# Kernel optimization log

Measured on AMD Instinct MI355X. Metric: run time of the kernel, lower is better.

Reference implementation:

```python
import jax, jax.numpy as jnp
import numpy as np

BATCH = 4
N_CTX = 1024
D_IN = 512
N_HEADS = 8
D_HEAD = 64
N_VARS = D_IN // D_HEAD  # ConstrainedRead default: n_vars = d_in // d_var = 8
TEMP = 1.0
ATTN_TEMP = float(np.sqrt(D_HEAD))  # attention_temp default = sqrt(d_head)


def setup_inputs() -> dict:
    key = jax.random.key(0)
    k1, k2, k3, k4, k5 = jax.random.split(key, 5)
    x = jax.random.uniform(k1, (BATCH, N_CTX, D_IN), dtype=jnp.float32)
    # causal tril mask, broadcast to batch (matches registered tril buffer usage)
    mask = jnp.broadcast_to(jnp.tril(jnp.ones((N_CTX, N_CTX), dtype=bool)), (BATCH, N_CTX, N_CTX))
    inv_sv = 1.0 / np.sqrt(N_VARS)
    W_K_W = jax.random.normal(k2, (N_HEADS, N_VARS), dtype=jnp.float32) * inv_sv
    W_Q_W = jax.random.normal(k3, (N_HEADS, N_VARS), dtype=jnp.float32) * inv_sv
    W_V_W = jax.random.normal(k4, (N_HEADS, N_VARS), dtype=jnp.float32) * inv_sv
    W_pred_W = jax.random.normal(k5, (N_HEADS, D_HEAD, D_HEAD), dtype=jnp.float32) / np.sqrt(D_HEAD)
    return {"x": x, "mask": mask, "W_K_W": W_K_W, "W_Q_W": W_Q_W, "W_V_W": W_V_W, "W_pred_W": W_pred_W}


def _constrained_read(W):
    # softmax over variables, then block-diagonal-style selector: (h, d_head, d_in)
    probs = jax.nn.softmax(W / TEMP, axis=-1)                 # (h, n_vars)
    eye = jnp.eye(D_HEAD, dtype=probs.dtype)                  # (c, c)
    rm = probs[:, :, None, None] * eye                        # (h, v, c, c)
    # einops 'a b c d -> a d (b c)'
    return jnp.transpose(rm, (0, 3, 1, 2)).reshape(N_HEADS, D_HEAD, D_IN)


def _fixed_bias_table():
    M = N_CTX  # table layout: [-2, linspace(0,-M,M-1)/M, linspace(-M,0,M)/M], shared over heads
    return jnp.concatenate([
        jnp.array([-2.0], dtype=jnp.float32),
        (jnp.linspace(0.0, -float(M), M - 1) / M).astype(jnp.float32),
        (jnp.linspace(-float(M), 0.0, M) / M).astype(jnp.float32),
    ])  # (2M,)


def reference(x, mask, W_K_W, W_Q_W, W_V_W, W_pred_W):
    WK = _constrained_read(W_K_W)
    WQm = _constrained_read(W_Q_W)
    WV = _constrained_read(W_V_W)
    # WPred: out[h,f,d] = sum_e W_Q[h,e,d] * softmax(W)[h,e,f]
    Wp = jax.nn.softmax(W_pred_W / TEMP, axis=-1)
    WQ = jnp.einsum('hed,hef->hfd', WQm, Wp)

    k = jnp.einsum('ihd,bpd->biph', WK, x)   # (b,h,p,dh)
    q = jnp.einsum('ihd,bpd->biph', WQ, x)
    v = jnp.einsum('ihd,bpd->biph', WV, x)

    pre = jnp.einsum('biph,biqh->biqp', k, q)            # (b,h,q,p)
    m = mask[:, None]                                    # (b,1,q,p)
    srow = jnp.where(m, pre, 0.0).sum(-1)                # (b,h,q)
    max_score = srow / (srow + 1e-10)
    pre = pre.at[:, :, :, 0].add(jax.nn.relu(1.0 - max_score))

    nq, nk = pre.shape[-2], pre.shape[-1]
    # relative position gather; %(2M) reproduces torch negative-index wraparound
    rel = (jnp.arange(nk)[None, :] - jnp.arange(nq)[:, None]) % (2 * N_CTX)
    bias = _fixed_bias_table()[rel]                      # (nq,nk), identical per head

    # one_hot_input=True: log(scores + 1e-20) + bias
    pos = jnp.log(pre + 1e-20) + bias[None, None]
    masked = jnp.where(m, pos, -1e30)
    attn = jax.nn.softmax(masked / ATTN_TEMP / TEMP, axis=-1)

    z = jnp.einsum('biph,biqp->biqh', v, attn)           # (b,h,q,dh)
    # einops 'b i q h -> b q (i h)'
    return jnp.transpose(z, (0, 2, 1, 3)).reshape(x.shape[0], nq, N_HEADS * D_HEAD)
```

## Files before the change

kernel.cpp:

```cpp
#include <hip/hip_runtime.h>
#include <math.h>

#define NCTX 1024
#define DIN 512
#define NH 8
#define DH 64

typedef float f32x16 __attribute__((ext_vector_type(16)));
typedef short bf16x8 __attribute__((ext_vector_type(8)));
typedef int i32x4 __attribute__((ext_vector_type(4)));

#define QF_OFF 0
#define KF_OFF (4u * 1024u * 1024u)
#define VF_OFF (8u * 1024u * 1024u)
#define V0_OFF (12u * 1024u * 1024u)

__device__ __forceinline__ bf16x8 asbf(i32x4 v) {
  union { i32x4 i; bf16x8 h; } u;
  u.i = v;
  return u.h;
}

__device__ __forceinline__ bf16x8 mk8(unsigned a, unsigned b, unsigned c,
                                      unsigned d) {
  union { unsigned u[4]; bf16x8 h; } x;
  x.u[0] = a; x.u[1] = b; x.u[2] = c; x.u[3] = d;
  return x.h;
}

__device__ __forceinline__ unsigned cvtpk(float lo, float hi_) {
  unsigned r;
  asm("v_cvt_pk_bf16_f32 %0, %1, %2" : "=v"(r) : "v"(lo), "v"(hi_));
  return r;
}

__device__ __forceinline__ void softmax8(const float* __restrict__ w,
                                         float* __restrict__ p) {
  float mx = w[0];
#pragma unroll
  for (int v = 1; v < 8; ++v) mx = fmaxf(mx, w[v]);
  float s = 0.f;
#pragma unroll
  for (int v = 0; v < 8; ++v) { p[v] = expf(w[v] - mx); s += p[v]; }
  const float inv = 1.f / s;
#pragma unroll
  for (int v = 0; v < 8; ++v) p[v] *= inv;
}

__global__ __launch_bounds__(256) void prep_kernel(
    const float* __restrict__ x, const float* __restrict__ WKw,
    const float* __restrict__ WQw, const float* __restrict__ WVw,
    const float* __restrict__ Wpred, short* __restrict__ Qf,
    short* __restrict__ Kf, short* __restrict__ Vf, float* __restrict__ V0f) {
  const int t = blockIdx.x, ih = blockIdx.y, b = blockIdx.z;
  const int bi = b * NH + ih;
  const int tid = threadIdx.x;

  __shared__ alignas(16) char smem[5 * 8192];
  char* const Ksb = smem;
  char* const Vtb = smem + 8192;
  char* const Q0b = smem + 16384;
  char* const WpT = smem + 24576;
  char* const Qsb = smem + 32768;

  {
    const int e = tid >> 2, sg = tid & 3;
    const float* wr = Wpred + (size_t)(ih * 64 + e) * 64 + sg * 16;
    float e16[16];
    float mx = -1e30f;
#pragma unroll
    for (int j = 0; j < 16; ++j) { e16[j] = wr[j]; mx = fmaxf(mx, e16[j]); }
    mx = fmaxf(mx, __shfl_xor(mx, 1, 4));
    mx = fmaxf(mx, __shfl_xor(mx, 2, 4));
    float s = 0.f;
#pragma unroll
    for (int j = 0; j < 16; ++j) { e16[j] = __expf(e16[j] - mx); s += e16[j]; }
    s += __shfl_xor(s, 1, 4);
    s += __shfl_xor(s, 2, 4);
    const float inv = 1.f / s;
#pragma unroll
    for (int j = 0; j < 16; ++j) {
      const int f = sg * 16 + j;
      const unsigned pz = cvtpk(e16[j] * inv, e16[j] * inv);
      *(unsigned short*)&WpT[f * 128 + ((2 * e) ^ ((f & 7) << 4))] =
          (unsigned short)pz;
    }
  }

  float pk[8], pq8[8], pv[8];
  {
    float w[8];
#pragma unroll
    for (int v = 0; v < 8; ++v) w[v] = WKw[ih * 8 + v];
    softmax8(w, pk);
#pragma unroll
    for (int v = 0; v < 8; ++v) w[v] = WQw[ih * 8 + v];
    softmax8(w, pq8);
#pragma unroll
    for (int v = 0; v < 8; ++v) w[v] = WVw[ih * 8 + v];
    softmax8(w, pv);
  }

  const int rg = tid >> 4, eg = tid & 15;
  const int r0 = rg * 4, e0 = eg * 4;
  float ka[4][4], qa[4][4], va[4][4];
#pragma unroll
  for (int i2 = 0; i2 < 4; ++i2)
#pragma unroll
    for (int j = 0; j < 4; ++j) { ka[i2][j] = 0.f; qa[i2][j] = 0.f; va[i2][j] = 0.f; }

  const float* xb = x + ((size_t)(b * NCTX + t * 64 + r0)) * DIN + e0;
#pragma unroll
  for (int v = 0; v < 8; ++v) {
#pragma unroll
    for (int i2 = 0; i2 < 4; ++i2) {
      const float4 xv = *(const float4*)(xb + (size_t)i2 * DIN + v * 64);
      ka[i2][0] = fmaf(pk[v], xv.x, ka[i2][0]);
      ka[i2][1] = fmaf(pk[v], xv.y, ka[i2][1]);
      ka[i2][2] = fmaf(pk[v], xv.z, ka[i2][2]);
      ka[i2][3] = fmaf(pk[v], xv.w, ka[i2][3]);
      qa[i2][0] = fmaf(pq8[v], xv.x, qa[i2][0]);
      qa[i2][1] = fmaf(pq8[v], xv.y, qa[i2][1]);
      qa[i2][2] = fmaf(pq8[v], xv.z, qa[i2][2]);
      qa[i2][3] = fmaf(pq8[v], xv.w, qa[i2][3]);
      va[i2][0] = fmaf(pv[v], xv.x, va[i2][0]);
      va[i2][1] = fmaf(pv[v], xv.y, va[i2][1]);
      va[i2][2] = fmaf(pv[v], xv.z, va[i2][2]);
      va[i2][3] = fmaf(pv[v], xv.w, va[i2][3]);
    }
  }

  if (t == 0 && rg == 0) {
    *(float4*)(V0f + bi * 64 + e0) =
        make_float4(va[0][0], va[0][1], va[0][2], va[0][3]);
  }

#pragma unroll
  for (int i2 = 0; i2 < 4; ++i2) {
    const int r = r0 + i2;
    const int boff = (2 * e0) ^ ((r & 7) << 4);
    *(uint2*)&Ksb[r * 128 + boff] =
        make_uint2(cvtpk(ka[i2][0], ka[i2][1]), cvtpk(ka[i2][2], ka[i2][3]));
    *(uint2*)&Q0b[r * 128 + boff] =
        make_uint2(cvtpk(qa[i2][0], qa[i2][1]), cvtpk(qa[i2][2], qa[i2][3]));
  }
#pragma unroll
  for (int j = 0; j < 4; ++j) {
    const int rr = e0 + j;
    *(uint2*)&Vtb[rr * 128 + ((2 * r0) ^ ((rr & 7) << 4))] =
        make_uint2(cvtpk(va[0][j], va[1][j]), cvtpk(va[2][j], va[3][j]));
  }
  __syncthreads();

  const int wv = tid >> 6;
  const int l = tid & 63;
  const int lm = l & 31;
  const int hi = l >> 5;

  const size_t fbase = (size_t)bi * 8192 + (size_t)t * 512;
#pragma unroll
  for (int c = 0; c < 2; ++c) {
    const int idx = c * 256 + tid;
    const int pq = idx >> 8, j = (idx >> 6) & 3, ll = idx & 63;
    const int krow = 32 * pq + (ll & 31);
    const i32x4 kfr = *(const i32x4*)
        &Ksb[krow * 128 + ((32 * j + 16 * (ll >> 5)) ^ ((krow & 7) << 4))];
    ((i32x4*)Kf)[fbase + idx] = kfr;
    const int vrow = 32 * (j & 1) + (ll & 31);
    const i32x4 vfr = *(const i32x4*)
        &Vtb[vrow * 128 +
             ((64 * pq + 32 * (j >> 1) + 16 * (ll >> 5)) ^ ((vrow & 7) << 4))];
    ((i32x4*)Vf)[fbase + idx] = vfr;
  }

  {
    const int qq = wv & 1, ff = wv >> 1;
    f32x16 dreg;
#pragma unroll
    for (int r = 0; r < 16; ++r) dreg[r] = 0.f;
    const int arow = 32 * qq + lm;
    const int brow = 32 * ff + lm;
#pragma unroll
    for (int kk = 0; kk < 4; ++kk) {
      const i32x4 af = *(const i32x4*)
          &Q0b[arow * 128 + ((32 * kk + 16 * hi) ^ ((arow & 7) << 4))];
      const i32x4 bfr = *(const i32x4*)
          &WpT[brow * 128 + ((32 * kk + 16 * hi) ^ ((brow & 7) << 4))];
      dreg = __builtin_amdgcn_mfma_f32_32x32x16_bf16(asbf(af), asbf(bfr),
                                                     dreg, 0, 0, 0);
    }
#pragma unroll
    for (int r = 0; r < 16; ++r) {
      const int q = 32 * qq + (r & 3) + 8 * (r >> 2) + 4 * hi;
      const int f = 32 * ff + lm;
      const unsigned pz = cvtpk(dreg[r], dreg[r]);
      *(unsigned short*)&Qsb[q * 128 + ((2 * f) ^ ((q & 7) << 4))] =
          (unsigned short)pz;
    }
  }
  __syncthreads();

#pragma unroll
  for (int c = 0; c < 2; ++c) {
    const int idx = c * 256 + tid;
    const int qq2 = idx >> 8, kk = (idx >> 6) & 3, ll = idx & 63;
    const int row = 32 * qq2 + (ll & 31);
    const i32x4 qfr = *(const i32x4*)
        &Qsb[row * 128 + ((32 * kk + 16 * (ll >> 5)) ^ ((row & 7) << 4))];
    ((i32x4*)Qf)[fbase + idx] = qfr;
  }
}

#if __has_builtin(__builtin_amdgcn_exp2f) && __has_builtin(__builtin_amdgcn_logf)
#define T_LOG(x) __builtin_amdgcn_logf(x)
#define T_EXP(x) __builtin_amdgcn_exp2f(x)
#define T_L 1.7628215e-4f
#define T_DIAG (-0.36067376f)
#else
#define T_LOG(x) __logf(x)
#define T_EXP(x) __expf(x)
#define T_L 1.2219941e-4f
#define T_DIAG (-0.25f)
#endif

__global__ __launch_bounds__(256, 2) void attn_kernel(
    const short* __restrict__ Qf, const short* __restrict__ Kf,
    const short* __restrict__ Vf, const float* __restrict__ V0f,
    float* __restrict__ out) {
  const int bx = blockIdx.x;
  const int a = bx >> 5;
  const int bi = bx & 31;
  const int qt = (a < 8) ? (15 - a) : (a - 8);
  const int b = bi >> 3, ih = bi & 7;
  const int tid = threadIdx.x;
  const int wv = tid >> 6;
  const int l = tid & 63;
  const int hi = l >> 5;
  const int lm = l & 31;
  const int pq = wv & 1;
  const int qq = wv >> 1;

  __shared__ float num_l[2][32][64];
  __shared__ float rdn[2][2][32];
  __shared__ float rsw[2][2][32];
  __shared__ float rp0[2][32];
  __shared__ float rdw[2][32];
  __shared__ float rinv[2][32];

  const i32x4* Qp = (const i32x4*)Qf + (size_t)bi * 8192 + (size_t)qt * 512 +
                    qq * 256;
  const i32x4* Kp = (const i32x4*)Kf + (size_t)bi * 8192 + pq * 256;
  const i32x4* Vp = (const i32x4*)Vf + (size_t)bi * 8192 + pq * 256;

  bf16x8 qfr[4];
#pragma unroll
  for (int kk = 0; kk < 4; ++kk) qfr[kk] = asbf(Qp[kk * 64 + l]);

  const float v0a = V0f[bi * 64 + lm];
  const float v0b = V0f[bi * 64 + 32 + lm];

  f32x16 num0, num1, stA, stB;
#pragma unroll
  for (int r = 0; r < 16; ++r) { num0[r] = 0.f; num1[r] = 0.f; }
  float den = 0.f, srw = 0.f, pre0 = 0.f;
  const int qg = qt * 64 + 32 * qq + lm;
  const int qpb = qg - 32 * pq - 4 * hi;

  i32x4 kA[4], vA[4], kB[4], vB[4];

#define LOADKV(PT, S)                                                   \
  do {                                                                  \
    const size_t o_ = (size_t)(PT) * 512;                               \
    _Pragma("unroll") for (int kk = 0; kk < 4; ++kk)                    \
        k##S[kk] = Kp[o_ + kk * 64 + l];                                \
    _Pragma("unroll") for (int j = 0; j < 4; ++j)                       \
        v##S[j] = Vp[o_ + j * 64 + l];                                  \
  } while (0)

#define QKSTEP(S)                                                            \
  do {                                                                       \
    _Pragma("unroll") for (int r = 0; r < 16; ++r) st##S[r] = 0.f;           \
    __builtin_amdgcn_s_setprio(1);                                           \
    _Pragma("unroll") for (int kk = 0; kk < 4; ++kk) st##S =                 \
        __builtin_amdgcn_mfma_f32_32x32x16_bf16(asbf(k##S[kk]), qfr[kk],     \
                                                st##S, 0, 0, 0);             \
    __builtin_amdgcn_s_setprio(0);                                           \
  } while (0)

#define PHASE(PT, CUR, NXT)                                                  \
  do {                                                                       \
    const int D0 = qpb - 64 * (PT);                                          \
    const float B0 = (1.0f - (float)D0) * T_L;                               \
    float w_[16];                                                            \
    _Pragma("unroll") for (int r = 0; r < 16; ++r) {                         \
      const int ro = (r & 3) + 8 * (r >> 2);                                 \
      const float pre = st##CUR[r];                                          \
      float b2 = B0 + (float)ro * T_L;                                       \
      b2 = (D0 == ro) ? T_DIAG : b2;                                         \
      b2 = (D0 < ro) ? -1e38f : b2;                                          \
      w_[r] = T_EXP(fmaf(0.125f, T_LOG(pre + 1e-20f), b2));                  \
      den += w_[r];                                                          \
      srw += (D0 >= ro) ? pre : 0.f;                                         \
    }                                                                        \
    if ((PT) == 0 && pq == 0 && hi == 0) pre0 = st##CUR[0];                  \
    if ((PT) + 1 <= qt) QKSTEP(NXT);                                         \
    const unsigned P0 = cvtpk(w_[0], w_[1]), P1 = cvtpk(w_[2], w_[3]);       \
    const unsigned P2 = cvtpk(w_[4], w_[5]), P3 = cvtpk(w_[6], w_[7]);       \
    const unsigned P4 = cvtpk(w_[8], w_[9]), P5 = cvtpk(w_[10], w_[11]);     \
    const unsigned P6 = cvtpk(w_[12], w_[13]), P7 = cvtpk(w_[14], w_[15]);   \
    const unsigned X0 = (unsigned)__shfl_xor((int)P0, 32, 64);               \
    const unsigned X1 = (unsigned)__shfl_xor((int)P1, 32, 64);               \
    const unsigned X2 = (unsigned)__shfl_xor((int)P2, 32, 64);               \
    const unsigned X3 = (unsigned)__shfl_xor((int)P3, 32, 64);               \
    const unsigned X4 = (unsigned)__shfl_xor((int)P4, 32, 64);               \
    const unsigned X5 = (unsigned)__shfl_xor((int)P5, 32, 64);               \
    const unsigned X6 = (unsigned)__shfl_xor((int)P6, 32, 64);               \
    const unsigned X7 = (unsigned)__shfl_xor((int)P7, 32, 64);               \
    const bool h1 = hi != 0;                                                 \
    const bf16x8 wf0 = mk8(h1 ? X2 : P0, h1 ? X3 : P1, h1 ? P2 : X0,         \
                           h1 ? P3 : X1);                                    \
    const bf16x8 wf1 = mk8(h1 ? X6 : P4, h1 ? X7 : P5, h1 ? P6 : X4,         \
                           h1 ? P7 : X5);                                    \
    __builtin_amdgcn_s_setprio(1);                                           \
    num0 = __builtin_amdgcn_mfma_f32_32x32x16_bf16(wf0, asbf(v##CUR[0]),     \
                                                   num0, 0, 0, 0);           \
    num1 = __builtin_amdgcn_mfma_f32_32x32x16_bf16(wf0, asbf(v##CUR[1]),     \
                                                   num1, 0, 0, 0);           \
    num0 = __builtin_amdgcn_mfma_f32_32x32x16_bf16(wf1, asbf(v##CUR[2]),     \
                                                   num0, 0, 0, 0);           \
    num1 = __builtin_amdgcn_mfma_f32_32x32x16_bf16(wf1, asbf(v##CUR[3]),     \
                                                   num1, 0, 0, 0);           \
    __builtin_amdgcn_s_setprio(0);                                           \
    if ((PT) + 2 <= qt) LOADKV((PT) + 2, CUR);                               \
  } while (0)

  LOADKV(0, A);
  QKSTEP(A);
  if (qt >= 1) LOADKV(1, B);
  for (int pt = 0; pt <= qt; pt += 2) {
    PHASE(pt, A, B);
    if (pt + 1 > qt) break;
    PHASE(pt + 1, B, A);
  }

  const float dsum = den + __shfl_xor(den, 32, 64);
  const float ssum = srw + __shfl_xor(srw, 32, 64);
  if (hi == 0) {
    rdn[qq][pq][lm] = dsum;
    rsw[qq][pq][lm] = ssum;
    if (pq == 0) rp0[qq][lm] = pre0;
  }
  if (pq == 1) {
#pragma unroll
    for (int r = 0; r < 16; ++r) {
      const int row = (r & 3) + 8 * (r >> 2) + 4 * hi;
      num_l[qq][row][lm] = num0[r];
      num_l[qq][row][32 + lm] = num1[r];
    }
  }
  __syncthreads();
  if (pq == 1 && hi == 0) {
    const int q = lm;
    const float dtot = rdn[qq][0][q] + rdn[qq][1][q];
    const float stot = rsw[qq][0][q] + rsw[qq][1][q];
    const float p0v = rp0[qq][q];
    const float ms = stot / (stot + 1e-10f);
    const float add = fmaxf(1.f - ms, 0.f);
    const int qgq = qt * 64 + qq * 32 + q;
    const float b8 =
        (qgq == 0) ? -0.25f : (1.0f - (float)qgq) * (0.125f / 1023.0f);
    const float w0n = __expf(fmaf(0.125f, __logf(p0v + add + 1e-20f), b8));
    const float w0o = __expf(fmaf(0.125f, __logf(p0v + 1e-20f), b8));
    const float dwv = w0n - w0o;
    rdw[qq][q] = dwv;
    rinv[qq][q] = 1.f / (dtot + dwv);
  }
  __syncthreads();
  if (pq == 0) {
#pragma unroll
    for (int r = 0; r < 16; ++r) {
      const int row = (r & 3) + 8 * (r >> 2) + 4 * hi;
      const int qgq = qt * 64 + qq * 32 + row;
      const float dwv = rdw[qq][row];
      const float iv = rinv[qq][row];
      const float o0 = (num0[r] + num_l[qq][row][lm] + dwv * v0a) * iv;
      const float o1 = (num1[r] + num_l[qq][row][32 + lm] + dwv * v0b) * iv;
      float* op = out + ((size_t)b * NCTX + qgq) * DIN + ih * DH;
      op[lm] = o0;
      op[32 + lm] = o1;
    }
  }
#undef LOADKV
#undef QKSTEP
#undef PHASE
}

extern "C" void kernel_launch(void* const* d_in, const int* in_sizes, int n_in,
                              void* d_out, int out_size, void* d_ws,
                              size_t ws_size, hipStream_t stream) {
  const float* x = (const float*)d_in[0];
  const float* WKw = (const float*)d_in[2];
  const float* WQw = (const float*)d_in[3];
  const float* WVw = (const float*)d_in[4];
  const float* Wpred = (const float*)d_in[5];
  float* out = (float*)d_out;

  short* Qf = (short*)((char*)d_ws + QF_OFF);
  short* Kf = (short*)((char*)d_ws + KF_OFF);
  short* Vf = (short*)((char*)d_ws + VF_OFF);
  float* V0f = (float*)((char*)d_ws + V0_OFF);

  dim3 block(256);
  dim3 grid1(16, NH, 4);
  hipLaunchKernelGGL(prep_kernel, grid1, block, 0, stream, x, WKw, WQw, WVw,
                     Wpred, Qf, Kf, Vf, V0f);
  dim3 grid2(512);
  hipLaunchKernelGGL(attn_kernel, grid2, block, 0, stream, Qf, Kf, Vf, V0f,
                     out);
}
```

Baseline: 31.78 us.

## Pair complementary causal query tiles in one 512-thread block for load balance

The attention kernel now launches 256 blocks of 512 threads, and each block processes two query tiles (qt and 15-qt) with separate wave groups. The two tiles have complementary causal lengths, so every block carries a near-equal amount of work and the grid tail is reduced. The next-tile QK MFMA is also issued before the current tile's softmax math rather than in the middle of it, and the den/srw accumulations are split into four partial sums to shorten dependency chains. Costs are doubled shared memory per block and possible register pressure under launch_bounds(512,2). Within a block, the wave group on the short tile still waits at the barriers for the group on the long tile.

```diff
diff --git a/kernel.cpp b/kernel.cpp
--- a/kernel.cpp
+++ b/kernel.cpp
@@ -223,29 +223,30 @@
 #define T_DIAG (-0.25f)
 #endif
 
-__global__ __launch_bounds__(256, 2) void attn_kernel(
+__global__ __launch_bounds__(512, 2) void attn_kernel(
     const short* __restrict__ Qf, const short* __restrict__ Kf,
     const short* __restrict__ Vf, const float* __restrict__ V0f,
     float* __restrict__ out) {
   const int bx = blockIdx.x;
-  const int a = bx >> 5;
+  const int P = bx >> 5;
   const int bi = bx & 31;
-  const int qt = (a < 8) ? (15 - a) : (a - 8);
   const int b = bi >> 3, ih = bi & 7;
   const int tid = threadIdx.x;
   const int wv = tid >> 6;
+  const int g = wv >> 2;
+  const int qt = g ? P : (15 - P);
   const int l = tid & 63;
   const int hi = l >> 5;
   const int lm = l & 31;
   const int pq = wv & 1;
-  const int qq = wv >> 1;
-
-  __shared__ float num_l[2][32][64];
-  __shared__ float rdn[2][2][32];
-  __shared__ float rsw[2][2][32];
-  __shared__ float rp0[2][32];
-  __shared__ float rdw[2][32];
-  __shared__ float rinv[2][32];
+  const int qq = (wv >> 1) & 1;
+
+  __shared__ float num_l[2][2][32][64];
+  __shared__ float rdn[2][2][2][32];
+  __shared__ float rsw[2][2][2][32];
+  __shared__ float rp0[2][2][32];
+  __shared__ float rdw[2][2][32];
+  __shared__ float rinv[2][2][32];
 
   const i32x4* Qp = (const i32x4*)Qf + (size_t)bi * 8192 + (size_t)qt * 512 +
                     qq * 256;
@@ -289,9 +290,12 @@
 
 #define PHASE(PT, CUR, NXT)                                                  \
   do {                                                                       \
+    if ((PT) + 1 <= qt) QKSTEP(NXT);                                         \
     const int D0 = qpb - 64 * (PT);                                          \
     const float B0 = (1.0f - (float)D0) * T_L;                               \
     float w_[16];                                                            \
+    float d4_[4] = {0.f, 0.f, 0.f, 0.f};                                     \
+    float s4_[4] = {0.f, 0.f, 0.f, 0.f};                                     \
     _Pragma("unroll") for (int r = 0; r < 16; ++r) {                         \
       const int ro = (r & 3) + 8 * (r >> 2);                                 \
       const float pre = st##CUR[r];                                          \
@@ -299,11 +303,12 @@
       b2 = (D0 == ro) ? T_DIAG : b2;                                         \
       b2 = (D0 < ro) ? -1e38f : b2;                                          \
       w_[r] = T_EXP(fmaf(0.125f, T_LOG(pre + 1e-20f), b2));                  \
-      den += w_[r];                                                          \
-      srw += (D0 >= ro) ? pre : 0.f;                                         \
+      d4_[r & 3] += w_[r];                                                   \
+      s4_[r & 3] += (D0 >= ro) ? pre : 0.f;                                  \
     }                                                                        \
+    den += (d4_[0] + d4_[1]) + (d4_[2] + d4_[3]);                            \
+    srw += (s4_[0] + s4_[1]) + (s4_[2] + s4_[3]);                            \
     if ((PT) == 0 && pq == 0 && hi == 0) pre0 = st##CUR[0];                  \
-    if ((PT) + 1 <= qt) QKSTEP(NXT);                                         \
     const unsigned P0 = cvtpk(w_[0], w_[1]), P1 = cvtpk(w_[2], w_[3]);       \
     const unsigned P2 = cvtpk(w_[4], w_[5]), P3 = cvtpk(w_[6], w_[7]);       \
     const unsigned P4 = cvtpk(w_[8], w_[9]), P5 = cvtpk(w_[10], w_[11]);     \
@@ -346,24 +351,24 @@
   const float dsum = den + __shfl_xor(den, 32, 64);
   const float ssum = srw + __shfl_xor(srw, 32, 64);
   if (hi == 0) {
-    rdn[qq][pq][lm] = dsum;
-    rsw[qq][pq][lm] = ssum;
-    if (pq == 0) rp0[qq][lm] = pre0;
+    rdn[g][qq][pq][lm] = dsum;
+    rsw[g][qq][pq][lm] = ssum;
+    if (pq == 0) rp0[g][qq][lm] = pre0;
   }
   if (pq == 1) {
 #pragma unroll
     for (int r = 0; r < 16; ++r) {
       const int row = (r & 3) + 8 * (r >> 2) + 4 * hi;
-      num_l[qq][row][lm] = num0[r];
-      num_l[qq][row][32 + lm] = num1[r];
+      num_l[g][qq][row][lm] = num0[r];
+      num_l[g][qq][row][32 + lm] = num1[r];
     }
   }
   __syncthreads();
   if (pq == 1 && hi == 0) {
     const int q = lm;
-    const float dtot = rdn[qq][0][q] + rdn[qq][1][q];
-    const float stot = rsw[qq][0][q] + rsw[qq][1][q];
-    const float p0v = rp0[qq][q];
+    const float dtot = rdn[g][qq][0][q] + rdn[g][qq][1][q];
+    const float stot = rsw[g][qq][0][q] + rsw[g][qq][1][q];
+    const float p0v = rp0[g][qq][q];
     const float ms = stot / (stot + 1e-10f);
     const float add = fmaxf(1.f - ms, 0.f);
     const int qgq = qt * 64 + qq * 32 + q;
@@ -372,8 +377,8 @@
     const float w0n = __expf(fmaf(0.125f, __logf(p0v + add + 1e-20f), b8));
     const float w0o = __expf(fmaf(0.125f, __logf(p0v + 1e-20f), b8));
     const float dwv = w0n - w0o;
-    rdw[qq][q] = dwv;
-    rinv[qq][q] = 1.f / (dtot + dwv);
+    rdw[g][qq][q] = dwv;
+    rinv[g][qq][q] = 1.f / (dtot + dwv);
   }
   __syncthreads();
   if (pq == 0) {
@@ -381,10 +386,10 @@
     for (int r = 0; r < 16; ++r) {
       const int row = (r & 3) + 8 * (r >> 2) + 4 * hi;
       const int qgq = qt * 64 + qq * 32 + row;
-      const float dwv = rdw[qq][row];
-      const float iv = rinv[qq][row];
-      const float o0 = (num0[r] + num_l[qq][row][lm] + dwv * v0a) * iv;
-      const float o1 = (num1[r] + num_l[qq][row][32 + lm] + dwv * v0b) * iv;
+      const float dwv = rdw[g][qq][row];
+      const float iv = rinv[g][qq][row];
+      const float o0 = (num0[r] + num_l[g][qq][row][lm] + dwv * v0a) * iv;
+      const float o1 = (num1[r] + num_l[g][qq][row][32 + lm] + dwv * v0b) * iv;
       float* op = out + ((size_t)b * NCTX + qgq) * DIN + ih * DH;
       op[lm] = o0;
       op[32 + lm] = o1;
@@ -414,7 +419,8 @@
   dim3 grid1(16, NH, 4);
   hipLaunchKernelGGL(prep_kernel, grid1, block, 0, stream, x, WKw, WQw, WVw,
                      Wpred, Qf, Kf, Vf, V0f);
-  dim3 grid2(512);
-  hipLaunchKernelGGL(attn_kernel, grid2, block, 0, stream, Qf, Kf, Vf, V0f,
+  dim3 block2(512);
+  dim3 grid2(256);
+  hipLaunchKernelGGL(attn_kernel, grid2, block2, 0, stream, Qf, Kf, Vf, V0f,
                      out);
 }
```

After: 31.87 us. About the same (+0.3%).

## Split attention blocks into 128-thread halves, specialize mask path, use permlane32 swap

Applied to the files above, without the earlier changes.

Each attention block now handles one 32-row query half with two waves instead of two halves with four waves, doubling the grid to 1024 blocks with an interleaved long/short tile schedule for load balance. The inner phase issues the next QK MFMA before the softmax math, skips mask/bias selection on non-diagonal tiles, and splits the den/srw reductions into four partial accumulators. The cross-half shuffle of packed bf16 weights is replaced with v_permlane32_swap instructions. The intent is finer-grained work distribution and less per-tile ALU/shuffle overhead, at the cost of smaller blocks and different occupancy bounds.

```diff
diff --git a/kernel.cpp b/kernel.cpp
--- a/kernel.cpp
+++ b/kernel.cpp
@@ -223,29 +223,34 @@
 #define T_DIAG (-0.25f)
 #endif
 
-__global__ __launch_bounds__(256, 2) void attn_kernel(
+__global__ __launch_bounds__(128, 3) void attn_kernel(
     const short* __restrict__ Qf, const short* __restrict__ Kf,
     const short* __restrict__ Vf, const float* __restrict__ V0f,
     float* __restrict__ out) {
   const int bx = blockIdx.x;
   const int a = bx >> 5;
   const int bi = bx & 31;
-  const int qt = (a < 8) ? (15 - a) : (a - 8);
+  const int s = a >> 1;
+  const int qhalf = a & 1;
+  const int s4 = s >> 2, sm = s & 3;
+  const int qt = (s4 == 0) ? (15 - 2 * sm)
+               : (s4 == 1) ? (2 * sm)
+               : (s4 == 2) ? (14 - 2 * sm)
+                           : (2 * sm + 1);
   const int b = bi >> 3, ih = bi & 7;
   const int tid = threadIdx.x;
-  const int wv = tid >> 6;
+  const int pq = tid >> 6;
   const int l = tid & 63;
   const int hi = l >> 5;
   const int lm = l & 31;
-  const int pq = wv & 1;
-  const int qq = wv >> 1;
-
-  __shared__ float num_l[2][32][64];
-  __shared__ float rdn[2][2][32];
-  __shared__ float rsw[2][2][32];
-  __shared__ float rp0[2][32];
-  __shared__ float rdw[2][32];
-  __shared__ float rinv[2][32];
+  const int qq = qhalf;
+
+  __shared__ float num_l[32][64];
+  __shared__ float rdn[2][32];
+  __shared__ float rsw[2][32];
+  __shared__ float rp0[32];
+  __shared__ float rdw[32];
+  __shared__ float rinv[32];
 
   const i32x4* Qp = (const i32x4*)Qf + (size_t)bi * 8192 + (size_t)qt * 512 +
                     qq * 256;
@@ -289,38 +294,48 @@
 
 #define PHASE(PT, CUR, NXT)                                                  \
   do {                                                                       \
+    if ((PT) + 1 <= qt) QKSTEP(NXT);                                         \
     const int D0 = qpb - 64 * (PT);                                          \
     const float B0 = (1.0f - (float)D0) * T_L;                               \
     float w_[16];                                                            \
-    _Pragma("unroll") for (int r = 0; r < 16; ++r) {                         \
-      const int ro = (r & 3) + 8 * (r >> 2);                                 \
-      const float pre = st##CUR[r];                                          \
-      float b2 = B0 + (float)ro * T_L;                                       \
-      b2 = (D0 == ro) ? T_DIAG : b2;                                         \
-      b2 = (D0 < ro) ? -1e38f : b2;                                          \
-      w_[r] = T_EXP(fmaf(0.125f, T_LOG(pre + 1e-20f), b2));                  \
-      den += w_[r];                                                          \
-      srw += (D0 >= ro) ? pre : 0.f;                                         \
+    float d4_[4] = {0.f, 0.f, 0.f, 0.f};                                     \
+    if ((PT) == qt) {                              \
+      float s4_[4] = {0.f, 0.f, 0.f, 0.f};                                   \
+      _Pragma("unroll") for (int r = 0; r < 16; ++r) {                       \
+        const int ro = (r & 3) + 8 * (r >> 2);                               \
+        const float pre = st##CUR[r];                                        \
+        float b2 = B0 + (float)ro * T_L;                                     \
+        b2 = (D0 == ro) ? T_DIAG : b2;                                       \
+        b2 = (D0 < ro) ? -1e38f : b2;                                        \
+        w_[r] = T_EXP(fmaf(0.125f, T_LOG(pre + 1e-20f), b2));                \
+        d4_[r & 3] += w_[r];                                                 \
+        s4_[r & 3] += (D0 >= ro) ? pre : 0.f;                                \
+      }                                                                      \
+      srw += (s4_[0] + s4_[1]) + (s4_[2] + s4_[3]);                          \
+    } else {                  \
+      float s4_[4] = {0.f, 0.f, 0.f, 0.f};                                   \
+      _Pragma("unroll") for (int r = 0; r < 16; ++r) {                       \
+        const int ro = (r & 3) + 8 * (r >> 2);                               \
+        const float pre = st##CUR[r];                                        \
+        const float b2 = B0 + (float)ro * T_L;                               \
+        w_[r] = T_EXP(fmaf(0.125f, T_LOG(pre + 1e-20f), b2));                \
+        d4_[r & 3] += w_[r];                                                 \
+        s4_[r & 3] += pre;                                                   \
+      }                                                                      \
+      srw += (s4_[0] + s4_[1]) + (s4_[2] + s4_[3]);                          \
     }                                                                        \
+    den += (d4_[0] + d4_[1]) + (d4_[2] + d4_[3]);                            \
     if ((PT) == 0 && pq == 0 && hi == 0) pre0 = st##CUR[0];                  \
-    if ((PT) + 1 <= qt) QKSTEP(NXT);                                         \
-    const unsigned P0 = cvtpk(w_[0], w_[1]), P1 = cvtpk(w_[2], w_[3]);       \
-    const unsigned P2 = cvtpk(w_[4], w_[5]), P3 = cvtpk(w_[6], w_[7]);       \
-    const unsigned P4 = cvtpk(w_[8], w_[9]), P5 = cvtpk(w_[10], w_[11]);     \
-    const unsigned P6 = cvtpk(w_[12], w_[13]), P7 = cvtpk(w_[14], w_[15]);   \
-    const unsigned X0 = (unsigned)__shfl_xor((int)P0, 32, 64);               \
-    const unsigned X1 = (unsigned)__shfl_xor((int)P1, 32, 64);               \
-    const unsigned X2 = (unsigned)__shfl_xor((int)P2, 32, 64);               \
-    const unsigned X3 = (unsigned)__shfl_xor((int)P3, 32, 64);               \
-    const unsigned X4 = (unsigned)__shfl_xor((int)P4, 32, 64);               \
-    const unsigned X5 = (unsigned)__shfl_xor((int)P5, 32, 64);               \
-    const unsigned X6 = (unsigned)__shfl_xor((int)P6, 32, 64);               \
-    const unsigned X7 = (unsigned)__shfl_xor((int)P7, 32, 64);               \
-    const bool h1 = hi != 0;                                                 \
-    const bf16x8 wf0 = mk8(h1 ? X2 : P0, h1 ? X3 : P1, h1 ? P2 : X0,         \
-                           h1 ? P3 : X1);                                    \
-    const bf16x8 wf1 = mk8(h1 ? X6 : P4, h1 ? X7 : P5, h1 ? P6 : X4,         \
-                           h1 ? P7 : X5);                                    \
+    unsigned P0 = cvtpk(w_[0], w_[1]), P1 = cvtpk(w_[2], w_[3]);             \
+    unsigned P2 = cvtpk(w_[4], w_[5]), P3 = cvtpk(w_[6], w_[7]);             \
+    unsigned P4 = cvtpk(w_[8], w_[9]), P5 = cvtpk(w_[10], w_[11]);           \
+    unsigned P6 = cvtpk(w_[12], w_[13]), P7 = cvtpk(w_[14], w_[15]);         \
+    asm("v_permlane32_swap_b32 %0, %1" : "+v"(P0), "+v"(P2));                \
+    asm("v_permlane32_swap_b32 %0, %1" : "+v"(P1), "+v"(P3));                \
+    asm("v_permlane32_swap_b32 %0, %1" : "+v"(P4), "+v"(P6));                \
+    asm("v_permlane32_swap_b32 %0, %1" : "+v"(P5), "+v"(P7));                \
+    const bf16x8 wf0 = mk8(P0, P1, P2, P3);                                  \
+    const bf16x8 wf1 = mk8(P4, P5, P6, P7);                                  \
     __builtin_amdgcn_s_setprio(1);                                           \
     num0 = __builtin_amdgcn_mfma_f32_32x32x16_bf16(wf0, asbf(v##CUR[0]),     \
                                                    num0, 0, 0, 0);           \
@@ -346,24 +361,24 @@
   const float dsum = den + __shfl_xor(den, 32, 64);
   const float ssum = srw + __shfl_xor(srw, 32, 64);
   if (hi == 0) {
-    rdn[qq][pq][lm] = dsum;
-    rsw[qq][pq][lm] = ssum;
-    if (pq == 0) rp0[qq][lm] = pre0;
+    rdn[pq][lm] = dsum;
+    rsw[pq][lm] = ssum;
+    if (pq == 0) rp0[lm] = pre0;
   }
   if (pq == 1) {
 #pragma unroll
     for (int r = 0; r < 16; ++r) {
       const int row = (r & 3) + 8 * (r >> 2) + 4 * hi;
-      num_l[qq][row][lm] = num0[r];
-      num_l[qq][row][32 + lm] = num1[r];
+      num_l[row][lm] = num0[r];
+      num_l[row][32 + lm] = num1[r];
     }
   }
   __syncthreads();
   if (pq == 1 && hi == 0) {
     const int q = lm;
-    const float dtot = rdn[qq][0][q] + rdn[qq][1][q];
-    const float stot = rsw[qq][0][q] + rsw[qq][1][q];
-    const float p0v = rp0[qq][q];
+    const float dtot = rdn[0][q] + rdn[1][q];
+    const float stot = rsw[0][q] + rsw[1][q];
+    const float p0v = rp0[q];
     const float ms = stot / (stot + 1e-10f);
     const float add = fmaxf(1.f - ms, 0.f);
     const int qgq = qt * 64 + qq * 32 + q;
@@ -372,8 +387,8 @@
     const float w0n = __expf(fmaf(0.125f, __logf(p0v + add + 1e-20f), b8));
     const float w0o = __expf(fmaf(0.125f, __logf(p0v + 1e-20f), b8));
     const float dwv = w0n - w0o;
-    rdw[qq][q] = dwv;
-    rinv[qq][q] = 1.f / (dtot + dwv);
+    rdw[q] = dwv;
+    rinv[q] = 1.f / (dtot + dwv);
   }
   __syncthreads();
   if (pq == 0) {
@@ -381,10 +396,10 @@
     for (int r = 0; r < 16; ++r) {
       const int row = (r & 3) + 8 * (r >> 2) + 4 * hi;
       const int qgq = qt * 64 + qq * 32 + row;
-      const float dwv = rdw[qq][row];
-      const float iv = rinv[qq][row];
-      const float o0 = (num0[r] + num_l[qq][row][lm] + dwv * v0a) * iv;
-      const float o1 = (num1[r] + num_l[qq][row][32 + lm] + dwv * v0b) * iv;
+      const float dwv = rdw[row];
+      const float iv = rinv[row];
+      const float o0 = (num0[r] + num_l[row][lm] + dwv * v0a) * iv;
+      const float o1 = (num1[r] + num_l[row][32 + lm] + dwv * v0b) * iv;
       float* op = out + ((size_t)b * NCTX + qgq) * DIN + ih * DH;
       op[lm] = o0;
       op[32 + lm] = o1;
@@ -414,7 +429,8 @@
   dim3 grid1(16, NH, 4);
   hipLaunchKernelGGL(prep_kernel, grid1, block, 0, stream, x, WKw, WQw, WVw,
                      Wpred, Qf, Kf, Vf, V0f);
-  dim3 grid2(512);
-  hipLaunchKernelGGL(attn_kernel, grid2, block, 0, stream, Qf, Kf, Vf, V0f,
+  dim3 block2(128);
+  dim3 grid2(1024);
+  hipLaunchKernelGGL(attn_kernel, grid2, block2, 0, stream, Qf, Kf, Vf, V0f,
                      out);
 }
```

After: 69.13 us. +117.6%, slower.
